# Kernel tuning notes

Hardware: AMD Instinct MI355X
Metric: run time of the kernel (lower is better)

Reference implementation:

```python
import jax, jax.numpy as jnp
import numpy as np

NUM_CLASSES = 120
IN_C = 512
FILTERS = 512

def setup_inputs() -> dict:
    key = jax.random.key(0)
    k1, k2, k3, k4 = jax.random.split(key, 4)
    B, H, W = 32, 64, 64
    x = jax.random.normal(k1, (B, H, W, IN_C), dtype=jnp.float32)
    cls = jax.random.randint(k2, (B, 1), 0, NUM_CLASSES, dtype=jnp.int64)
    # kernel table: (num_classes, 1, 1, in_c, filters), glorot-like scale
    scale = (2.0 / (IN_C + FILTERS)) ** 0.5
    kernel = jax.random.normal(k3, (NUM_CLASSES, 1, 1, IN_C, FILTERS), dtype=jnp.float32) * scale
    bias = jnp.zeros((NUM_CLASSES, FILTERS), dtype=jnp.float32)
    return {"x": x, "cls": cls, "kernel": kernel, "bias": bias}

def reference(x, cls, kernel, bias):
    # x: [B,H,W,C] (channels_last), cls: [B,1] int ids
    c = jnp.squeeze(cls, axis=1)                      # [B]
    w = kernel[c, 0, 0]                               # [B, C, F] gathered per-sample kernel
    b = bias[c]                                       # [B, F]
    # per-sample 1x1 conv == batched matmul over pixels
    out = jnp.einsum('bhwc,bcf->bhwf', x, w)          # [B,H,W,F]
    out = out + b[:, None, None, :]
    return out
```

## Files before the change

### kernel.cpp

```cpp
#include <hip/hip_runtime.h>
#include <hip/hip_bf16.h>

typedef __bf16 bf16_t;
typedef __bf16 bf16x4 __attribute__((ext_vector_type(4)));
typedef __bf16 bf16x8 __attribute__((ext_vector_type(8)));
typedef float  f32x4  __attribute__((ext_vector_type(4)));

#define NB      32
#define NPIX    4096
#define CIN     512
#define FOUT    512
#define TM      128
#define TN      128
#define BK      32
#define LDPAD   40

__global__ __launch_bounds__(256) void gather_w_kernel(
    const float* __restrict__ kern, const int* __restrict__ cls,
    bf16_t* __restrict__ wsB)
{
    __shared__ float tile[32][33];
    const int n0 = blockIdx.x * 32;
    const int k0 = blockIdx.y * 32;
    const int b  = blockIdx.z;
    const int c  = cls[b];
    const int tx = threadIdx.x;
    const int ty = threadIdx.y;

    const float* src = kern + (long)c * CIN * FOUT;
#pragma unroll
    for (int i = 0; i < 4; i++) {
        int k = k0 + ty + i * 8;
        tile[ty + i * 8][tx] = src[(long)k * FOUT + n0 + tx];
    }
    __syncthreads();
    bf16_t* dst = wsB + (long)b * FOUT * CIN;
#pragma unroll
    for (int i = 0; i < 4; i++) {
        int n = n0 + ty + i * 8;
        dst[(long)n * CIN + k0 + tx] = (bf16_t)tile[tx][ty + i * 8];
    }
}

__global__ __launch_bounds__(256) void cond_conv_gemm(
    const float*  __restrict__ x,
    const bf16_t* __restrict__ wsB,
    const float*  __restrict__ bias,
    const int*    __restrict__ cls,
    float*        __restrict__ out)
{
    __shared__ bf16_t As[TM * LDPAD];
    __shared__ bf16_t Bs[TN * LDPAD];

    const int bid = blockIdx.x;
    const int n_t = bid & 3;
    const int m_t = (bid >> 2) & 31;
    const int b   = bid >> 7;

    const long x_base = (long)b * NPIX * CIN + (long)m_t * TM * CIN;
    const long w_base = (long)b * FOUT * CIN;
    const int  n0     = n_t * TN;

    const int t    = threadIdx.x;
    const int wave = t >> 6;
    const int lane = t & 63;
    const int wm   = (wave >> 1) * 64;
    const int wn   = (wave & 1) * 64;
    const int l15  = lane & 15;
    const int quad = lane >> 4;

    f32x4 acc[4][4];
#pragma unroll
    for (int i = 0; i < 4; i++)
#pragma unroll
        for (int j = 0; j < 4; j++)
            acc[i][j] = (f32x4){0.f, 0.f, 0.f, 0.f};

    for (int k0 = 0; k0 < CIN; k0 += BK) {
#pragma unroll
        for (int g = 0; g < 4; g++) {
            int chunk = t + g * 256;
            int m  = chunk >> 3;
            int kc = (chunk & 7) << 2;
            float4 v = *(const float4*)(x + x_base + (long)m * CIN + k0 + kc);
            bf16x4 h;
            h[0] = (bf16_t)v.x; h[1] = (bf16_t)v.y;
            h[2] = (bf16_t)v.z; h[3] = (bf16_t)v.w;
            *(bf16x4*)(&As[m * LDPAD + kc]) = h;
        }
#pragma unroll
        for (int g = 0; g < 2; g++) {
            int chunk = t + g * 256;
            int n  = chunk >> 2;
            int kc = (chunk & 3) << 3;
            bf16x8 v = *(const bf16x8*)(wsB + w_base + (long)(n0 + n) * CIN + k0 + kc);
            *(bf16x8*)(&Bs[n * LDPAD + kc]) = v;
        }
        __syncthreads();

        bf16x8 af[4], bf[4];
#pragma unroll
        for (int i = 0; i < 4; i++)
            af[i] = *(const bf16x8*)(&As[(wm + i * 16 + l15) * LDPAD + quad * 8]);
#pragma unroll
        for (int i = 0; i < 4; i++)
            bf[i] = *(const bf16x8*)(&Bs[(wn + i * 16 + l15) * LDPAD + quad * 8]);
#pragma unroll
        for (int mi = 0; mi < 4; mi++)
#pragma unroll
            for (int ni = 0; ni < 4; ni++)
                acc[mi][ni] = __builtin_amdgcn_mfma_f32_16x16x32_bf16(
                    af[mi], bf[ni], acc[mi][ni], 0, 0, 0);
        __syncthreads();
    }

    const int c = cls[b];
    const long out_base = (long)b * NPIX * FOUT + (long)(m_t * TM) * FOUT + n0;
#pragma unroll
    for (int ni = 0; ni < 4; ni++) {
        float bv = bias[(long)c * FOUT + n0 + wn + ni * 16 + l15];
        int col = wn + ni * 16 + l15;
#pragma unroll
        for (int mi = 0; mi < 4; mi++) {
#pragma unroll
            for (int r = 0; r < 4; r++) {
                int row = wm + mi * 16 + quad * 4 + r;
                out[out_base + (long)row * FOUT + col] = acc[mi][ni][r] + bv;
            }
        }
    }
}

__global__ __launch_bounds__(256) void naive_kernel(
    const float* __restrict__ x, const float* __restrict__ kern,
    const float* __restrict__ bias, const int* __restrict__ cls,
    float* __restrict__ out)
{
    long i = (long)blockIdx.x * 256 + threadIdx.x;
    if (i >= (long)NB * NPIX * FOUT) return;
    int f = (int)(i % FOUT);
    long p = i / FOUT;
    int b = (int)(p / NPIX);
    int c = cls[b];
    const float* xr = x + p * CIN;
    const float* wc = kern + (long)c * CIN * FOUT + f;
    float acc = 0.f;
    for (int k = 0; k < CIN; k++) acc += xr[k] * wc[(long)k * FOUT];
    out[i] = acc + bias[(long)c * FOUT + f];
}

extern "C" void kernel_launch(void* const* d_in, const int* in_sizes, int n_in,
                              void* d_out, int out_size, void* d_ws, size_t ws_size,
                              hipStream_t stream)
{
    const float* x    = (const float*)d_in[0];
    const int*   cls  = (const int*)d_in[1];
    const float* kern = (const float*)d_in[2];
    const float* bias = (const float*)d_in[3];
    float*       out  = (float*)d_out;

    const size_t ws_need = (size_t)NB * FOUT * CIN * sizeof(bf16_t);
    if (ws_size >= ws_need) {
        bf16_t* wsB = (bf16_t*)d_ws;
        gather_w_kernel<<<dim3(FOUT / 32, CIN / 32, NB), dim3(32, 8), 0, stream>>>(
            kern, cls, wsB);
        cond_conv_gemm<<<NB * (NPIX / TM) * (FOUT / TN), 256, 0, stream>>>(
            x, wsB, bias, cls, out);
    } else {
        long n = (long)NB * NPIX * FOUT;
        naive_kernel<<<(int)((n + 255) / 256), 256, 0, stream>>>(x, kern, bias, cls, out);
    }
}
```

Baseline: 616.5 us.

## Pre-convert x to bf16 and load GEMM tiles directly into LDS

Adds a pass that converts the fp32 activations to bf16 in workspace. A new GEMM kernel then loads both operand tiles with global_load_lds (direct global-to-LDS DMA) into unpadded shared memory, replacing register-staged loads and in-loop conversion. The intent is to cut per-tile global traffic and VALU conversion work inside the GEMM, at the cost of an extra full read and write of x (about 256MB in, 128MB out). Unpadded LDS rows may also cause bank conflicts on the fragment reads.

```diff
diff --git a/kernel.cpp b/kernel.cpp
--- a/kernel.cpp
+++ b/kernel.cpp
@@ -5,6 +5,7 @@
 typedef __bf16 bf16x4 __attribute__((ext_vector_type(4)));
 typedef __bf16 bf16x8 __attribute__((ext_vector_type(8)));
 typedef float  f32x4  __attribute__((ext_vector_type(4)));
+typedef unsigned int u32;
 
 #define NB      32
 #define NPIX    4096
@@ -15,6 +16,17 @@
 #define BK      32
 #define LDPAD   40
 
+__global__ __launch_bounds__(256) void cvt_x_kernel(
+    const float* __restrict__ x, bf16_t* __restrict__ xb)
+{
+    long i = ((long)blockIdx.x * 256 + threadIdx.x) * 4;
+    float4 v = *(const float4*)(x + i);
+    bf16x4 h;
+    h[0] = (bf16_t)v.x; h[1] = (bf16_t)v.y;
+    h[2] = (bf16_t)v.z; h[3] = (bf16_t)v.w;
+    *(bf16x4*)(xb + i) = h;
+}
+
 __global__ __launch_bounds__(256) void gather_w_kernel(
     const float* __restrict__ kern, const int* __restrict__ cls,
     bf16_t* __restrict__ wsB)
@@ -39,6 +51,96 @@
     for (int i = 0; i < 4; i++) {
         int n = n0 + ty + i * 8;
         dst[(long)n * CIN + k0 + tx] = (bf16_t)tile[tx][ty + i * 8];
+    }
+}
+
+__global__ __launch_bounds__(256) void cond_gemm_bf16(
+    const bf16_t* __restrict__ xb,
+    const bf16_t* __restrict__ wsB,
+    const float*  __restrict__ bias,
+    const int*    __restrict__ cls,
+    float*        __restrict__ out)
+{
+    __shared__ bf16_t As[TM * BK];
+    __shared__ bf16_t Bs[TN * BK];
+
+    const int bid = blockIdx.x;
+    const int n_t = bid & 3;
+    const int m_t = (bid >> 2) & 31;
+    const int b   = bid >> 7;
+
+    const long x_base = (long)b * NPIX * CIN + (long)m_t * TM * CIN;
+    const long w_base = (long)b * FOUT * CIN + (long)n_t * TN * CIN;
+
+    const int t    = threadIdx.x;
+    const int wave = t >> 6;
+    const int lane = t & 63;
+    const int wm   = (wave >> 1) * 64;
+    const int wn   = (wave & 1) * 64;
+    const int l15  = lane & 15;
+    const int quad = lane >> 4;
+
+    const int srow  = lane >> 2;
+    const int skoff = (lane & 3) * 8;
+
+    f32x4 acc[4][4];
+#pragma unroll
+    for (int i = 0; i < 4; i++)
+#pragma unroll
+        for (int j = 0; j < 4; j++)
+            acc[i][j] = (f32x4){0.f, 0.f, 0.f, 0.f};
+
+    for (int k0 = 0; k0 < CIN; k0 += BK) {
+#pragma unroll
+        for (int j = 0; j < 2; j++) {
+            const int rbase = wave * 32 + j * 16;
+            const bf16_t* g = xb + x_base + (long)(rbase + srow) * CIN + k0 + skoff;
+            bf16_t* l = As + rbase * BK;
+            __builtin_amdgcn_global_load_lds(
+                (const __attribute__((address_space(1))) u32*)g,
+                (__attribute__((address_space(3))) u32*)l, 16, 0, 0);
+        }
+#pragma unroll
+        for (int j = 0; j < 2; j++) {
+            const int rbase = wave * 32 + j * 16;
+            const bf16_t* g = wsB + w_base + (long)(rbase + srow) * CIN + k0 + skoff;
+            bf16_t* l = Bs + rbase * BK;
+            __builtin_amdgcn_global_load_lds(
+                (const __attribute__((address_space(1))) u32*)g,
+                (__attribute__((address_space(3))) u32*)l, 16, 0, 0);
+        }
+        __syncthreads();
+
+        bf16x8 af[4], bf[4];
+#pragma unroll
+        for (int i = 0; i < 4; i++)
+            af[i] = *(const bf16x8*)(&As[(wm + i * 16 + l15) * BK + quad * 8]);
+#pragma unroll
+        for (int i = 0; i < 4; i++)
+            bf[i] = *(const bf16x8*)(&Bs[(wn + i * 16 + l15) * BK + quad * 8]);
+#pragma unroll
+        for (int mi = 0; mi < 4; mi++)
+#pragma unroll
+            for (int ni = 0; ni < 4; ni++)
+                acc[mi][ni] = __builtin_amdgcn_mfma_f32_16x16x32_bf16(
+                    af[mi], bf[ni], acc[mi][ni], 0, 0, 0);
+        __syncthreads();
+    }
+
+    const int c = cls[b];
+    const long out_base = (long)b * NPIX * FOUT + (long)(m_t * TM) * FOUT + n_t * TN;
+#pragma unroll
+    for (int ni = 0; ni < 4; ni++) {
+        int col = wn + ni * 16 + l15;
+        float bv = bias[(long)c * FOUT + n_t * TN + col];
+#pragma unroll
+        for (int mi = 0; mi < 4; mi++) {
+#pragma unroll
+            for (int r = 0; r < 4; r++) {
+                int row = wm + mi * 16 + quad * 4 + r;
+                out[out_base + (long)row * FOUT + col] = acc[mi][ni][r] + bv;
+            }
+        }
     }
 }
 
@@ -159,8 +261,19 @@
     const float* bias = (const float*)d_in[3];
     float*       out  = (float*)d_out;
 
-    const size_t ws_need = (size_t)NB * FOUT * CIN * sizeof(bf16_t);
-    if (ws_size >= ws_need) {
+    const size_t xb_bytes = (size_t)NB * NPIX * CIN * sizeof(bf16_t);
+    const size_t w_bytes  = (size_t)NB * FOUT * CIN * sizeof(bf16_t);
+
+    if (ws_size >= xb_bytes + w_bytes) {
+        bf16_t* xb  = (bf16_t*)d_ws;
+        bf16_t* wsB = (bf16_t*)((char*)d_ws + xb_bytes);
+        long nelem = (long)NB * NPIX * CIN;
+        cvt_x_kernel<<<(int)(nelem / (256 * 4)), 256, 0, stream>>>(x, xb);
+        gather_w_kernel<<<dim3(FOUT / 32, CIN / 32, NB), dim3(32, 8), 0, stream>>>(
+            kern, cls, wsB);
+        cond_gemm_bf16<<<NB * (NPIX / TM) * (FOUT / TN), 256, 0, stream>>>(
+            xb, wsB, bias, cls, out);
+    } else if (ws_size >= w_bytes) {
         bf16_t* wsB = (bf16_t*)d_ws;
         gather_w_kernel<<<dim3(FOUT / 32, CIN / 32, NB), dim3(32, 8), 0, stream>>>(
             kern, cls, wsB);
```

Result: no change. 627.8 us (+1.8%).
